# Kernel tuning notes

Hardware: AMD Instinct MI355X
Metric: run time of the kernel (lower is better)

## Reference

```python
import jax, jax.numpy as jnp
import numpy as np


def _lstm(x, W, U, b, return_sequences):
    # x: [B,T,F]; W: [F,4H]; U: [H,4H]; b: [4H]. Keras gate order: i,f,c,o.
    B = x.shape[0]
    H = U.shape[0]
    # precompute input projection for all timesteps: [T,B,4H]
    xW = jnp.einsum('btf,fg->tbg', x, W) + b
    h0 = jnp.zeros((B, H), x.dtype)
    c0 = jnp.zeros((B, H), x.dtype)

    def step(carry, xw):
        h, c = carry
        z = xw + h @ U  # [B,4H]
        i, f, g, o = jnp.split(z, 4, axis=-1)
        i = jax.nn.sigmoid(i)
        f = jax.nn.sigmoid(f)
        g = jax.nn.relu(g)      # activation='relu' on candidate
        o = jax.nn.sigmoid(o)
        c = f * c + i * g
        h = o * jax.nn.relu(c)  # activation='relu' on cell output
        return (h, c), h

    (hT, _), hs = jax.lax.scan(step, (h0, c0), xW)
    if return_sequences:
        return jnp.transpose(hs, (1, 0, 2))  # [B,T,H]
    return hT  # [B,H]


def setup_inputs() -> dict:
    key = jax.random.key(0)
    ks = jax.random.split(key, 11)
    B, T, F = 512, 512, 64
    H1, H2, D1, D2 = 128, 64, 25, 1
    s = 0.05  # small weight scale keeps the relu-LSTM recurrence numerically stable
    return {
        'x':   jax.random.normal(ks[0], (B, T, F), jnp.float32),
        'W1':  jax.random.normal(ks[1], (F, 4 * H1), jnp.float32) * s,
        'U1':  jax.random.normal(ks[2], (H1, 4 * H1), jnp.float32) * s,
        'b1':  jnp.zeros((4 * H1,), jnp.float32),
        'W2':  jax.random.normal(ks[3], (H1, 4 * H2), jnp.float32) * s,
        'U2':  jax.random.normal(ks[4], (H2, 4 * H2), jnp.float32) * s,
        'b2':  jnp.zeros((4 * H2,), jnp.float32),
        'Wd1': jax.random.normal(ks[5], (H2, D1), jnp.float32) * s,
        'bd1': jnp.zeros((D1,), jnp.float32),
        'Wd2': jax.random.normal(ks[6], (D1, D2), jnp.float32) * s,
        'bd2': jnp.zeros((D2,), jnp.float32),
    }


def reference(x, W1, U1, b1, W2, U2, b2, Wd1, bd1, Wd2, bd2):
    h = _lstm(x, W1, U1, b1, return_sequences=True)   # [B,T,128]
    h = _lstm(h, W2, U2, b2, return_sequences=False)  # [B,64]
    h = h @ Wd1 + bd1                                  # [B,25]
    return h @ Wd2 + bd2                               # [B,1]
```

## Files before the change

### kernel.cpp

```cpp
#include <hip/hip_runtime.h>
#include <type_traits>

typedef _Float16 f16;
typedef _Float16 f16x4 __attribute__((ext_vector_type(4)));
typedef _Float16 f16x8 __attribute__((ext_vector_type(8)));
typedef float    f32x4 __attribute__((ext_vector_type(4)));

constexpr int TT = 512;
constexpr int FF = 64;
constexpr int H1 = 128;
constexpr int H2 = 64;
constexpr int D1 = 25;
constexpr int S1 = 136;
constexpr int S2 = 72;
constexpr int XC = 8;
constexpr float L2E = 1.44269504088896f;

__device__ __forceinline__ float sigm2(float z) {
    return __builtin_amdgcn_rcpf(1.f + __builtin_amdgcn_exp2f(-z));
}

__device__ __forceinline__ f32x4 mfma16(f16x8 a, f16x8 b, f32x4 c) {
    return __builtin_amdgcn_mfma_f32_16x16x32_f16(a, b, c, 0, 0, 0);
}

__device__ __forceinline__ void gl_lds16(const f16* g, f16* l) {
    __builtin_amdgcn_global_load_lds(
        (const __attribute__((address_space(1))) unsigned int*)g,
        (__attribute__((address_space(3))) unsigned int*)l, 16, 0, 0);
}

__global__ void cvt_x_kernel(const float* __restrict__ x, f16* __restrict__ xh) {
    const size_t i = ((size_t)blockIdx.x * blockDim.x + threadIdx.x) * 4;
    const float4 v = *(const float4*)(x + i);
    f16x4 h; h[0] = (f16)v.x; h[1] = (f16)v.y; h[2] = (f16)v.z; h[3] = (f16)v.w;
    *(f16x4*)(xh + i) = h;
}

__global__ __launch_bounds__(768, 3)
void lstm_pipe5(const f16* __restrict__ xh, const float* __restrict__ W1,
                const float* __restrict__ U1, const float* __restrict__ b1,
                const float* __restrict__ W2, const float* __restrict__ U2,
                const float* __restrict__ b2, const float* __restrict__ Wd1,
                const float* __restrict__ bd1,const float* __restrict__ Wd2,
                const float* __restrict__ bd2, float* __restrict__ out)
{
    const int tid  = threadIdx.x;
    const int w    = tid >> 6;
    const int lane = tid & 63;
    const int quad = lane >> 4;
    const int lid  = lane & 15;
    const int b0   = blockIdx.x * 16;
    const bool isL1 = (w < 8);
    const int  j    = isL1 ? w : (w - 8);

    __shared__ __align__(16) f16 h1b[2][16][S1];
    __shared__ __align__(16) f16 h2b[2][16][S2];
    __shared__ __align__(16) f16 xlds[2][XC * 8 * 16 * 8];
    __shared__ float h2f[16][H2];
    __shared__ float dsh[16][D1];

    for (int i = tid; i < 2 * 16 * S1 / 2; i += 768) ((unsigned*)h1b)[i] = 0u;
    for (int i = tid; i < 2 * 16 * S2 / 2; i += 768) ((unsigned*)h2b)[i] = 0u;

    for (int s = tid; s < XC * 8 * 16; s += 768) {
        const int tl = s >> 7, fs = (s >> 4) & 7, row = s & 15;
        const f16* gp = xh + ((size_t)(b0 + row) * TT + tl) * FF + fs * 8;
        gl_lds16(gp, &xlds[0][(s >> 6) * 512]);
    }

    f16x8 wt[4][6];
    f32x4 bsp[4];
    float cs[4] = {0.f, 0.f, 0.f, 0.f};

    if (isL1) {
#pragma unroll
        for (int g = 0; g < 4; ++g) {
            const float sc = (g == 2) ? 1.f : L2E;
            const int n = 128 * g + 16 * w + lid;
            const float bb = b1[n] * sc;
            bsp[g][0] = bb; bsp[g][1] = bb; bsp[g][2] = bb; bsp[g][3] = bb;
#pragma unroll
            for (int c = 0; c < 4; ++c) {
                f16x8 f;
#pragma unroll
                for (int e = 0; e < 8; ++e)
                    f[e] = (f16)(U1[(32 * c + quad * 8 + e) * 512 + n] * sc);
                wt[g][c] = f;
            }
#pragma unroll
            for (int c = 0; c < 2; ++c) {
                f16x8 f;
#pragma unroll
                for (int e = 0; e < 8; ++e)
                    f[e] = (f16)(W1[(32 * c + quad * 8 + e) * 512 + n] * sc);
                wt[g][4 + c] = f;
            }
        }
    } else {
#pragma unroll
        for (int g = 0; g < 4; ++g) {
            const float sc = (g == 2) ? 1.f : L2E;
            const int n = 64 * g + 16 * j + lid;
            const float bb = b2[n] * sc;
            bsp[g][0] = bb; bsp[g][1] = bb; bsp[g][2] = bb; bsp[g][3] = bb;
#pragma unroll
            for (int c = 0; c < 4; ++c) {
                f16x8 f;
#pragma unroll
                for (int e = 0; e < 8; ++e)
                    f[e] = (f16)(W2[(32 * c + quad * 8 + e) * 256 + n] * sc);
                wt[g][c] = f;
            }
#pragma unroll
            for (int c = 0; c < 2; ++c) {
                f16x8 f;
#pragma unroll
                for (int e = 0; e < 8; ++e)
                    f[e] = (f16)(U2[(32 * c + quad * 8 + e) * 256 + n] * sc);
                wt[g][4 + c] = f;
            }
        }
    }
    __syncthreads();

    auto step = [&](auto parc, int i) {
        constexpr int PAR = decltype(parc)::value;
        constexpr int PR = PAR ^ 1;
        constexpr int PW = PAR;
        constexpr int QR = PAR;
        constexpr int QW = PAR ^ 1;
        if (isL1) {
            const f16* xc = &xlds[(i >> 3) & 1][(i & 7) * 1024];
            f16x8 fr0 = *(const f16x8*)&h1b[PR][lid][quad * 8];
            f16x8 fr1 = *(const f16x8*)&h1b[PR][lid][32 + quad * 8];
            f16x8 fr2 = *(const f16x8*)&h1b[PR][lid][64 + quad * 8];
            f16x8 fr3 = *(const f16x8*)&h1b[PR][lid][96 + quad * 8];
            f16x8 xf0 = *(const f16x8*)&xc[(quad * 16 + lid) * 8];
            f16x8 xf1 = *(const f16x8*)&xc[((4 + quad) * 16 + lid) * 8];
            f32x4 acc[4];
#pragma unroll
            for (int g = 0; g < 4; ++g) {
                f32x4 a = mfma16(fr0, wt[g][0], bsp[g]);
                a = mfma16(fr1, wt[g][1], a);
                a = mfma16(fr2, wt[g][2], a);
                a = mfma16(fr3, wt[g][3], a);
                a = mfma16(xf0, wt[g][4], a);
                a = mfma16(xf1, wt[g][5], a);
                acc[g] = a;
            }
#pragma unroll
            for (int r = 0; r < 4; ++r) {
                const float ig = sigm2(acc[0][r]);
                const float fg = sigm2(acc[1][r]);
                const float gg = fmaxf(acc[2][r], 0.f);
                const float og = sigm2(acc[3][r]);
                const float cc = fg * cs[r] + ig * gg;
                cs[r] = cc;
                const float hv = og * fmaxf(cc, 0.f);
                h1b[PW][quad * 4 + r][16 * w + lid] = (f16)hv;
            }
        } else {
            if (i >= 1) {
                f16x8 fr0 = *(const f16x8*)&h1b[PR][lid][quad * 8];
                f16x8 fr1 = *(const f16x8*)&h1b[PR][lid][32 + quad * 8];
                f16x8 fr2 = *(const f16x8*)&h1b[PR][lid][64 + quad * 8];
                f16x8 fr3 = *(const f16x8*)&h1b[PR][lid][96 + quad * 8];
                f16x8 fr4 = *(const f16x8*)&h2b[QR][lid][quad * 8];
                f16x8 fr5 = *(const f16x8*)&h2b[QR][lid][32 + quad * 8];
                f32x4 acc[4];
#pragma unroll
                for (int g = 0; g < 4; ++g) {
                    f32x4 a = mfma16(fr0, wt[g][0], bsp[g]);
                    a = mfma16(fr1, wt[g][1], a);
                    a = mfma16(fr2, wt[g][2], a);
                    a = mfma16(fr3, wt[g][3], a);
                    a = mfma16(fr4, wt[g][4], a);
                    a = mfma16(fr5, wt[g][5], a);
                    acc[g] = a;
                }
#pragma unroll
                for (int r = 0; r < 4; ++r) {
                    const float ig = sigm2(acc[0][r]);
                    const float fg = sigm2(acc[1][r]);
                    const float gg = fmaxf(acc[2][r], 0.f);
                    const float og = sigm2(acc[3][r]);
                    const float cc = fg * cs[r] + ig * gg;
                    cs[r] = cc;
                    const float hv = og * fmaxf(cc, 0.f);
                    h2b[QW][quad * 4 + r][16 * j + lid] = (f16)hv;
                }
            }
        }
    };

    for (int ii = 0; ii < TT; ii += 2) {
        if ((ii & (XC - 1)) == 0 && ii + XC < TT) {
            const int nc = (ii >> 3) + 1;
            f16* dst = xlds[nc & 1];
            for (int s = tid; s < XC * 8 * 16; s += 768) {
                const int tl = s >> 7, fs = (s >> 4) & 7, row = s & 15;
                const f16* gp = xh + ((size_t)(b0 + row) * TT + (nc * XC + tl)) * FF + fs * 8;
                gl_lds16(gp, &dst[(s >> 6) * 512]);
            }
        }
        step(std::integral_constant<int, 0>{}, ii);
        __syncthreads();
        step(std::integral_constant<int, 1>{}, ii + 1);
        __syncthreads();
    }

    if (!isL1) {
        f16x8 fr0 = *(const f16x8*)&h1b[1][lid][quad * 8];
        f16x8 fr1 = *(const f16x8*)&h1b[1][lid][32 + quad * 8];
        f16x8 fr2 = *(const f16x8*)&h1b[1][lid][64 + quad * 8];
        f16x8 fr3 = *(const f16x8*)&h1b[1][lid][96 + quad * 8];
        f16x8 fr4 = *(const f16x8*)&h2b[0][lid][quad * 8];
        f16x8 fr5 = *(const f16x8*)&h2b[0][lid][32 + quad * 8];
        f32x4 acc[4];
#pragma unroll
        for (int g = 0; g < 4; ++g) {
            f32x4 a = mfma16(fr0, wt[g][0], bsp[g]);
            a = mfma16(fr1, wt[g][1], a);
            a = mfma16(fr2, wt[g][2], a);
            a = mfma16(fr3, wt[g][3], a);
            a = mfma16(fr4, wt[g][4], a);
            a = mfma16(fr5, wt[g][5], a);
            acc[g] = a;
        }
#pragma unroll
        for (int r = 0; r < 4; ++r) {
            const float ig = sigm2(acc[0][r]);
            const float fg = sigm2(acc[1][r]);
            const float gg = fmaxf(acc[2][r], 0.f);
            const float og = sigm2(acc[3][r]);
            const float cc = fg * cs[r] + ig * gg;
            const float hv = og * fmaxf(cc, 0.f);
            h2f[quad * 4 + r][16 * j + lid] = hv;
        }
    }
    __syncthreads();

    for (int idx = tid; idx < 16 * D1; idx += 768) {
        const int bq = idx / D1, p = idx % D1;
        float d = bd1[p];
#pragma unroll
        for (int k = 0; k < H2; ++k) d += h2f[bq][k] * Wd1[k * D1 + p];
        dsh[bq][p] = d * Wd2[p];
    }
    __syncthreads();
    if (tid < 16) {
        float o = bd2[0];
#pragma unroll
        for (int p = 0; p < D1; ++p) o += dsh[tid][p];
        out[b0 + tid] = o;
    }
}

extern "C" void kernel_launch(void* const* d_in, const int* in_sizes, int n_in,
                              void* d_out, int out_size, void* d_ws, size_t ws_size,
                              hipStream_t stream) {
    (void)in_sizes; (void)n_in; (void)out_size; (void)ws_size;
    const float* x   = (const float*)d_in[0];
    const float* W1  = (const float*)d_in[1];
    const float* U1  = (const float*)d_in[2];
    const float* b1  = (const float*)d_in[3];
    const float* W2  = (const float*)d_in[4];
    const float* U2  = (const float*)d_in[5];
    const float* b2  = (const float*)d_in[6];
    const float* Wd1 = (const float*)d_in[7];
    const float* bd1 = (const float*)d_in[8];
    const float* Wd2 = (const float*)d_in[9];
    const float* bd2 = (const float*)d_in[10];
    float* out = (float*)d_out;
    f16*   xh  = (f16*)d_ws;

    const int nx = 512 * 512 * 64;
    cvt_x_kernel<<<dim3(nx / (256 * 4)), dim3(256), 0, stream>>>(x, xh);
    lstm_pipe5<<<dim3(32), dim3(768), 0, stream>>>(
        xh, W1, U1, b1, W2, U2, b2, Wd1, bd1, Wd2, bd2, out);
}
```

Baseline: 749.3 us.

## Shrink block to 8 waves with each layer-1 wave computing two column tiles

Reassigns work so 4 waves handle layer 1, each owning two 16-column hidden tiles, and 4 waves handle layer 2, dropping the block from 12 waves to 8. Biases move from MFMA accumulator initialisation to scalar adds after the MFMA chain. The aim is to reduce per-step barrier cost and wave count on the serial recurrence. In exchange, layer-1 waves hold twice the weight registers and do twice the MFMA and gate work per step, which lengthens their part of the critical path.

```diff
diff --git a/kernel.cpp b/kernel.cpp
--- a/kernel.cpp
+++ b/kernel.cpp
@@ -37,8 +37,8 @@
     *(f16x4*)(xh + i) = h;
 }
 
-__global__ __launch_bounds__(768, 3)
-void lstm_pipe5(const f16* __restrict__ xh, const float* __restrict__ W1,
+__global__ __launch_bounds__(512, 2)
+void lstm_pipe6(const f16* __restrict__ xh, const float* __restrict__ W1,
                 const float* __restrict__ U1, const float* __restrict__ b1,
                 const float* __restrict__ W2, const float* __restrict__ U2,
                 const float* __restrict__ b2, const float* __restrict__ Wd1,
@@ -51,8 +51,9 @@
     const int quad = lane >> 4;
     const int lid  = lane & 15;
     const int b0   = blockIdx.x * 16;
-    const bool isL1 = (w < 8);
-    const int  j    = isL1 ? w : (w - 8);
+    const bool isL1 = (w >= 4);
+    const int  w1   = w - 4;
+    const int  w2   = w;
 
     __shared__ __align__(16) f16 h1b[2][16][S1];
     __shared__ __align__(16) f16 h2b[2][16][S2];
@@ -60,65 +61,70 @@
     __shared__ float h2f[16][H2];
     __shared__ float dsh[16][D1];
 
-    for (int i = tid; i < 2 * 16 * S1 / 2; i += 768) ((unsigned*)h1b)[i] = 0u;
-    for (int i = tid; i < 2 * 16 * S2 / 2; i += 768) ((unsigned*)h2b)[i] = 0u;
-
-    for (int s = tid; s < XC * 8 * 16; s += 768) {
-        const int tl = s >> 7, fs = (s >> 4) & 7, row = s & 15;
-        const f16* gp = xh + ((size_t)(b0 + row) * TT + tl) * FF + fs * 8;
-        gl_lds16(gp, &xlds[0][(s >> 6) * 512]);
-    }
-
-    f16x8 wt[4][6];
-    f32x4 bsp[4];
-    float cs[4] = {0.f, 0.f, 0.f, 0.f};
+    for (int i = tid; i < 2 * 16 * S1 / 2; i += 512) ((unsigned*)h1b)[i] = 0u;
+    for (int i = tid; i < 2 * 16 * S2 / 2; i += 512) ((unsigned*)h2b)[i] = 0u;
+
+    if (tid < 256) {
+        for (int s = tid; s < XC * 8 * 16; s += 256) {
+            const int tl = s >> 7, fs = (s >> 4) & 7, row = s & 15;
+            const f16* gp = xh + ((size_t)(b0 + row) * TT + tl) * FF + fs * 8;
+            gl_lds16(gp, &xlds[0][(s >> 6) * 512]);
+        }
+    }
+
+    f16x8 wt1[2][4][6];
+    f16x8 wt2[4][6];
+    float bias1[2][4], bias2[4];
+    float cs1[8] = {0,0,0,0,0,0,0,0};
+    float cs2[4] = {0,0,0,0};
 
     if (isL1) {
+#pragma unroll
+        for (int h = 0; h < 2; ++h) {
+#pragma unroll
+            for (int g = 0; g < 4; ++g) {
+                const float sc = (g == 2) ? 1.f : L2E;
+                const int n = 128 * g + 32 * w1 + 16 * h + lid;
+                bias1[h][g] = b1[n] * sc;
+#pragma unroll
+                for (int c = 0; c < 4; ++c) {
+                    f16x8 f;
+#pragma unroll
+                    for (int e = 0; e < 8; ++e)
+                        f[e] = (f16)(U1[(32 * c + quad * 8 + e) * 512 + n] * sc);
+                    wt1[h][g][c] = f;
+                }
+#pragma unroll
+                for (int c = 0; c < 2; ++c) {
+                    f16x8 f;
+#pragma unroll
+                    for (int e = 0; e < 8; ++e)
+                        f[e] = (f16)(W1[(32 * c + quad * 8 + e) * 512 + n] * sc);
+                    wt1[h][g][4 + c] = f;
+                }
+            }
+        }
+    } else {
 #pragma unroll
         for (int g = 0; g < 4; ++g) {
             const float sc = (g == 2) ? 1.f : L2E;
-            const int n = 128 * g + 16 * w + lid;
-            const float bb = b1[n] * sc;
-            bsp[g][0] = bb; bsp[g][1] = bb; bsp[g][2] = bb; bsp[g][3] = bb;
+            const int n = 64 * g + 16 * w2 + lid;
+            bias2[g] = b2[n] * sc;
 #pragma unroll
             for (int c = 0; c < 4; ++c) {
                 f16x8 f;
 #pragma unroll
                 for (int e = 0; e < 8; ++e)
-                    f[e] = (f16)(U1[(32 * c + quad * 8 + e) * 512 + n] * sc);
-                wt[g][c] = f;
+                    f[e] = (f16)(W2[(32 * c + quad * 8 + e) * 256 + n] * sc);
+                wt2[g][c] = f;
             }
 #pragma unroll
             for (int c = 0; c < 2; ++c) {
                 f16x8 f;
 #pragma unroll
                 for (int e = 0; e < 8; ++e)
-                    f[e] = (f16)(W1[(32 * c + quad * 8 + e) * 512 + n] * sc);
-                wt[g][4 + c] = f;
-            }
-        }
-    } else {
-#pragma unroll
-        for (int g = 0; g < 4; ++g) {
-            const float sc = (g == 2) ? 1.f : L2E;
-            const int n = 64 * g + 16 * j + lid;
-            const float bb = b2[n] * sc;
-            bsp[g][0] = bb; bsp[g][1] = bb; bsp[g][2] = bb; bsp[g][3] = bb;
-#pragma unroll
-            for (int c = 0; c < 4; ++c) {
-                f16x8 f;
-#pragma unroll
-                for (int e = 0; e < 8; ++e)
-                    f[e] = (f16)(W2[(32 * c + quad * 8 + e) * 256 + n] * sc);
-                wt[g][c] = f;
-            }
-#pragma unroll
-            for (int c = 0; c < 2; ++c) {
-                f16x8 f;
-#pragma unroll
-                for (int e = 0; e < 8; ++e)
                     f[e] = (f16)(U2[(32 * c + quad * 8 + e) * 256 + n] * sc);
-                wt[g][4 + c] = f;
+                wt2[g][4 + c] = f;
             }
         }
     }
@@ -138,27 +144,31 @@
             f16x8 fr3 = *(const f16x8*)&h1b[PR][lid][96 + quad * 8];
             f16x8 xf0 = *(const f16x8*)&xc[(quad * 16 + lid) * 8];
             f16x8 xf1 = *(const f16x8*)&xc[((4 + quad) * 16 + lid) * 8];
-            f32x4 acc[4];
-#pragma unroll
-            for (int g = 0; g < 4; ++g) {
-                f32x4 a = mfma16(fr0, wt[g][0], bsp[g]);
-                a = mfma16(fr1, wt[g][1], a);
-                a = mfma16(fr2, wt[g][2], a);
-                a = mfma16(fr3, wt[g][3], a);
-                a = mfma16(xf0, wt[g][4], a);
-                a = mfma16(xf1, wt[g][5], a);
-                acc[g] = a;
-            }
-#pragma unroll
-            for (int r = 0; r < 4; ++r) {
-                const float ig = sigm2(acc[0][r]);
-                const float fg = sigm2(acc[1][r]);
-                const float gg = fmaxf(acc[2][r], 0.f);
-                const float og = sigm2(acc[3][r]);
-                const float cc = fg * cs[r] + ig * gg;
-                cs[r] = cc;
-                const float hv = og * fmaxf(cc, 0.f);
-                h1b[PW][quad * 4 + r][16 * w + lid] = (f16)hv;
+#pragma unroll
+            for (int h = 0; h < 2; ++h) {
+                f32x4 acc[4];
+#pragma unroll
+                for (int g = 0; g < 4; ++g) {
+                    f32x4 a = {0.f, 0.f, 0.f, 0.f};
+                    a = mfma16(fr0, wt1[h][g][0], a);
+                    a = mfma16(fr1, wt1[h][g][1], a);
+                    a = mfma16(fr2, wt1[h][g][2], a);
+                    a = mfma16(fr3, wt1[h][g][3], a);
+                    a = mfma16(xf0, wt1[h][g][4], a);
+                    a = mfma16(xf1, wt1[h][g][5], a);
+                    acc[g] = a;
+                }
+#pragma unroll
+                for (int r = 0; r < 4; ++r) {
+                    const float ig = sigm2(acc[0][r] + bias1[h][0]);
+                    const float fg = sigm2(acc[1][r] + bias1[h][1]);
+                    const float gg = fmaxf(acc[2][r] + bias1[h][2], 0.f);
+                    const float og = sigm2(acc[3][r] + bias1[h][3]);
+                    const float cc = fg * cs1[h * 4 + r] + ig * gg;
+                    cs1[h * 4 + r] = cc;
+                    const float hv = og * fmaxf(cc, 0.f);
+                    h1b[PW][quad * 4 + r][32 * w1 + 16 * h + lid] = (f16)hv;
+                }
             }
         } else {
             if (i >= 1) {
@@ -171,34 +181,35 @@
                 f32x4 acc[4];
 #pragma unroll
                 for (int g = 0; g < 4; ++g) {
-                    f32x4 a = mfma16(fr0, wt[g][0], bsp[g]);
-                    a = mfma16(fr1, wt[g][1], a);
-                    a = mfma16(fr2, wt[g][2], a);
-                    a = mfma16(fr3, wt[g][3], a);
-                    a = mfma16(fr4, wt[g][4], a);
-                    a = mfma16(fr5, wt[g][5], a);
+                    f32x4 a = {0.f, 0.f, 0.f, 0.f};
+                    a = mfma16(fr0, wt2[g][0], a);
+                    a = mfma16(fr1, wt2[g][1], a);
+                    a = mfma16(fr2, wt2[g][2], a);
+                    a = mfma16(fr3, wt2[g][3], a);
+                    a = mfma16(fr4, wt2[g][4], a);
+                    a = mfma16(fr5, wt2[g][5], a);
                     acc[g] = a;
                 }
 #pragma unroll
                 for (int r = 0; r < 4; ++r) {
-                    const float ig = sigm2(acc[0][r]);
-                    const float fg = sigm2(acc[1][r]);
-                    const float gg = fmaxf(acc[2][r], 0.f);
-                    const float og = sigm2(acc[3][r]);
-                    const float cc = fg * cs[r] + ig * gg;
-                    cs[r] = cc;
+                    const float ig = sigm2(acc[0][r] + bias2[0]);
+                    const float fg = sigm2(acc[1][r] + bias2[1]);
+                    const float gg = fmaxf(acc[2][r] + bias2[2], 0.f);
+                    const float og = sigm2(acc[3][r] + bias2[3]);
+                    const float cc = fg * cs2[r] + ig * gg;
+                    cs2[r] = cc;
                     const float hv = og * fmaxf(cc, 0.f);
-                    h2b[QW][quad * 4 + r][16 * j + lid] = (f16)hv;
+                    h2b[QW][quad * 4 + r][16 * w2 + lid] = (f16)hv;
                 }
             }
         }
     };
 
     for (int ii = 0; ii < TT; ii += 2) {
-        if ((ii & (XC - 1)) == 0 && ii + XC < TT) {
+        if ((ii & (XC - 1)) == 0 && ii + XC < TT && tid < 256) {
             const int nc = (ii >> 3) + 1;
             f16* dst = xlds[nc & 1];
-            for (int s = tid; s < XC * 8 * 16; s += 768) {
+            for (int s = tid; s < XC * 8 * 16; s += 256) {
                 const int tl = s >> 7, fs = (s >> 4) & 7, row = s & 15;
                 const f16* gp = xh + ((size_t)(b0 + row) * TT + (nc * XC + tl)) * FF + fs * 8;
                 gl_lds16(gp, &dst[(s >> 6) * 512]);
@@ -220,28 +231,29 @@
         f32x4 acc[4];
 #pragma unroll
         for (int g = 0; g < 4; ++g) {
-            f32x4 a = mfma16(fr0, wt[g][0], bsp[g]);
-            a = mfma16(fr1, wt[g][1], a);
-            a = mfma16(fr2, wt[g][2], a);
-            a = mfma16(fr3, wt[g][3], a);
-            a = mfma16(fr4, wt[g][4], a);
-            a = mfma16(fr5, wt[g][5], a);
+            f32x4 a = {0.f, 0.f, 0.f, 0.f};
+            a = mfma16(fr0, wt2[g][0], a);
+            a = mfma16(fr1, wt2[g][1], a);
+            a = mfma16(fr2, wt2[g][2], a);
+            a = mfma16(fr3, wt2[g][3], a);
+            a = mfma16(fr4, wt2[g][4], a);
+            a = mfma16(fr5, wt2[g][5], a);
             acc[g] = a;
         }
 #pragma unroll
         for (int r = 0; r < 4; ++r) {
-            const float ig = sigm2(acc[0][r]);
-            const float fg = sigm2(acc[1][r]);
-            const float gg = fmaxf(acc[2][r], 0.f);
-            const float og = sigm2(acc[3][r]);
-            const float cc = fg * cs[r] + ig * gg;
+            const float ig = sigm2(acc[0][r] + bias2[0]);
+            const float fg = sigm2(acc[1][r] + bias2[1]);
+            const float gg = fmaxf(acc[2][r] + bias2[2], 0.f);
+            const float og = sigm2(acc[3][r] + bias2[3]);
+            const float cc = fg * cs2[r] + ig * gg;
             const float hv = og * fmaxf(cc, 0.f);
-            h2f[quad * 4 + r][16 * j + lid] = hv;
+            h2f[quad * 4 + r][16 * w2 + lid] = hv;
         }
     }
     __syncthreads();
 
-    for (int idx = tid; idx < 16 * D1; idx += 768) {
+    for (int idx = tid; idx < 16 * D1; idx += 512) {
         const int bq = idx / D1, p = idx % D1;
         float d = bd1[p];
 #pragma unroll
@@ -277,6 +289,6 @@
 
     const int nx = 512 * 512 * 64;
     cvt_x_kernel<<<dim3(nx / (256 * 4)), dim3(256), 0, stream>>>(x, xh);
-    lstm_pipe5<<<dim3(32), dim3(768), 0, stream>>>(
+    lstm_pipe6<<<dim3(32), dim3(512), 0, stream>>>(
         xh, W1, U1, b1, W2, U2, b2, Wd1, bd1, Wd2, bd2, out);
 }
```

Result: slower. 2.237 ms (+198.5%).
